# Performance work log

Measured on AMD Instinct MI355X. Metric: run time of the kernel, lower is better.

## Reference

```python
import jax, jax.numpy as jnp
import numpy as np

IN_CH = 768
FH = FW = 14                      # hardcoded feature grid in the module
SCALES = (128.0, 256.0, 512.0)
RATIOS = (0.5, 1.0, 2.0)
A = len(SCALES) * len(RATIOS)     # 9 anchors / location
PRENMS_TOPK = 1000
NMS_THRESH = 0.7
TOPK = 300
MIN_SIZE = 16.0
BBOX_XFORM_CLIP = float(np.log(1000.0 / 16.0))


def generate_anchors(img_h, img_w):
    scales = jnp.asarray(SCALES, jnp.float32)
    ratios = jnp.asarray(RATIOS, jnp.float32)
    h_r = jnp.sqrt(ratios)
    w_r = 1.0 / h_r
    ws = (w_r[:, None] * scales[None, :]).reshape(-1)   # aspect-major, scale-minor
    hs = (h_r[:, None] * scales[None, :]).reshape(-1)
    base = jnp.round(jnp.stack([-ws, -hs, ws, hs], axis=1) / 2.0)  # [A,4]
    stride_h, stride_w = img_h // FH, img_w // FW
    sx = (jnp.arange(FW) * stride_w).astype(jnp.float32)
    sy = (jnp.arange(FH) * stride_h).astype(jnp.float32)
    yy, xx = jnp.meshgrid(sy, sx, indexing='ij')
    shifts = jnp.stack([xx, yy, xx, yy], axis=-1).reshape(-1, 4)   # [H*W,4]
    return (shifts[:, None, :] + base[None, :, :]).reshape(-1, 4)  # [H*W*A,4]


def decode_boxes(deltas, anchors):
    w = anchors[:, 2] - anchors[:, 0]
    h = anchors[:, 3] - anchors[:, 1]
    cx = anchors[:, 0] + 0.5 * w
    cy = anchors[:, 1] + 0.5 * h
    dx, dy = deltas[:, 0], deltas[:, 1]
    dw = jnp.minimum(deltas[:, 2], BBOX_XFORM_CLIP)
    dh = jnp.minimum(deltas[:, 3], BBOX_XFORM_CLIP)
    pcx = dx * w + cx
    pcy = dy * h + cy
    pw = jnp.exp(dw) * w
    ph = jnp.exp(dh) * h
    return jnp.stack([pcx - 0.5 * pw, pcy - 0.5 * ph,
                      pcx + 0.5 * pw, pcy + 0.5 * ph], axis=1)


def nms_keep(boxes, valid, thresh):
    # boxes sorted by descending score; greedy NMS. valid marks boxes that
    # survived the min-size filter.
    area = (boxes[:, 2] - boxes[:, 0]) * (boxes[:, 3] - boxes[:, 1])
    lt = jnp.maximum(boxes[:, None, :2], boxes[None, :, :2])
    rb = jnp.minimum(boxes[:, None, 2:], boxes[None, :, 2:])
    wh = jnp.clip(rb - lt, 0.0)
    inter = wh[..., 0] * wh[..., 1]
    union = area[:, None] + area[None, :] - inter
    iou = jnp.where(union > 0, inter / union, 0.0)   # [N,N]
    n = boxes.shape[0]
    order = jnp.arange(n)

    def body(i, keep):
        sup = (iou[i] > thresh) & keep[i] & (order > i)
        return keep & ~sup

    return jax.lax.fori_loop(0, n, body, valid)


def rpn_forward(image, feature, w_conv, b_conv, w_cls, b_cls, w_reg, b_reg):
    # feature: [1,197,768] -> drop CLS -> raw reshape to [1,768,14,14]
    feat = feature[:, 1:, :].reshape(1, IN_CH, FH, FW)
    x = jax.lax.conv_general_dilated(
        feat, w_conv, window_strides=(1, 1), padding='SAME',
        dimension_numbers=('NCHW', 'OIHW', 'NCHW')) + b_conv[None, :, None, None]
    x = jax.nn.relu(x)
    # 1x1 heads as einsum
    cls = jnp.einsum('nchw,oc->nohw', x, w_cls[:, :, 0, 0]) + b_cls[None, :, None, None]
    reg = jnp.einsum('nchw,oc->nohw', x, w_reg[:, :, 0, 0]) + b_reg[None, :, None, None]
    # [1,A,H,W] -> [H*W*A] (location-major, anchor-minor)
    scores = cls.transpose(0, 2, 3, 1).reshape(-1)
    # [1,4A,H,W] -> [1,A,4,H,W] -> [1,H,W,A,4] -> [H*W*A,4]
    deltas = reg.reshape(1, A, 4, FH, FW).transpose(0, 3, 4, 1, 2).reshape(-1, 4)

    img_h, img_w = image.shape[2], image.shape[3]
    anchors = generate_anchors(img_h, img_w)
    proposals = decode_boxes(deltas, anchors)

    # filter_proposals: sigmoid -> prenms topk -> clip -> min-size -> NMS -> topk
    probs = jax.nn.sigmoid(scores)
    k = min(PRENMS_TOPK, probs.shape[0])
    top_scores, idx = jax.lax.top_k(probs, k)
    boxes = proposals[idx]
    boxes = jnp.stack([jnp.clip(boxes[:, 0], 0.0, img_w),
                       jnp.clip(boxes[:, 1], 0.0, img_h),
                       jnp.clip(boxes[:, 2], 0.0, img_w),
                       jnp.clip(boxes[:, 3], 0.0, img_h)], axis=1)
    ws = boxes[:, 2] - boxes[:, 0]
    hs = boxes[:, 3] - boxes[:, 1]
    valid = (ws >= MIN_SIZE) & (hs >= MIN_SIZE)
    keep = nms_keep(boxes, valid, NMS_THRESH)

    masked = jnp.where(keep, top_scores, -1.0)   # sigmoid scores are > 0
    out_scores, oidx = jax.lax.top_k(masked, TOPK)
    out_boxes = boxes[oidx]
    pad = out_scores > 0.0                        # suppressed slots -> zero pad
    out_boxes = out_boxes * pad[:, None]
    out_scores = out_scores * pad
    return out_boxes, out_scores                  # [TOPK,4], [TOPK]


def setup_inputs() -> dict:
    key = jax.random.key(0)
    ks = jax.random.split(key, 6)
    return {
        'image': jax.random.normal(ks[0], (1, 3, 224, 224), jnp.float32),
        'feature': jax.random.normal(ks[1], (1, 197, IN_CH), jnp.float32),
        'w_conv': 0.01 * jax.random.normal(ks[2], (IN_CH, IN_CH, 3, 3), jnp.float32),
        'b_conv': jnp.zeros((IN_CH,), jnp.float32),
        'w_cls': 0.01 * jax.random.normal(ks[3], (A, IN_CH, 1, 1), jnp.float32),
        'b_cls': jnp.zeros((A,), jnp.float32),
        'w_reg': 0.01 * jax.random.normal(ks[4], (4 * A, IN_CH, 1, 1), jnp.float32),
        'b_reg': jnp.zeros((4 * A,), jnp.float32),
    }


def reference(image, feature, w_conv, b_conv, w_cls, b_cls, w_reg, b_reg):
    return rpn_forward(image, feature, w_conv, b_conv, w_cls, b_cls, w_reg, b_reg)
```

## Files before the change

kernel.cpp:

```cpp
#include <hip/hip_runtime.h>
#include <cstdint>
#include <cstddef>

#define IN_CH 768
#define FH 14
#define FW 14
#define NPOS 196
#define NA 9
#define NANCH 1764
#define K1 1000
#define TOPK_N 300
#define CSPLIT 16
#define CPBLK (IN_CH / CSPLIT)
#define WCH (CPBLK / 4)
#define HQ 8
#define HCC (IN_CH / HQ)
#define BBOX_CLIP 4.135166556742356f
#define IMG_W 224.0f
#define IMG_H 224.0f

typedef unsigned long long ull;

__device__ __forceinline__ uint32_t f2sort(float f) {
    uint32_t b = __float_as_uint(f);
    return (b & 0x80000000u) ? ~b : (b | 0x80000000u);
}
__device__ __forceinline__ float sort2f(uint32_t s) {
    uint32_t b = (s & 0x80000000u) ? (s & 0x7fffffffu) : ~s;
    return __uint_as_float(b);
}
__device__ __forceinline__ ull readlane_u64(ull v, int l) {
    unsigned lo = __builtin_amdgcn_readlane((unsigned)(v & 0xffffffffull), l);
    unsigned hi = __builtin_amdgcn_readlane((unsigned)(v >> 32), l);
    return ((ull)hi << 32) | (ull)lo;
}

__global__ __launch_bounds__(256) void k_pad(const float* __restrict__ feature,
                                             float* __restrict__ pad) {
    const int c = blockIdx.x, t = threadIdx.x;
    const int row = t >> 4, col = t & 15;
    const bool in = (row >= 1 && row <= 14 && col >= 1 && col <= 14);
    pad[(size_t)c * 256 + t] = in ? feature[IN_CH + (size_t)c * NPOS + (row - 1) * FW + (col - 1)] : 0.f;
}

__global__ __launch_bounds__(256) void k_conv(const float* __restrict__ pad,
                                              const float* __restrict__ w_conv,
                                              float* __restrict__ xpart) {
    __shared__ float wlds[CPBLK * 8 * 12];
    const int tid  = threadIdx.x;
    const int wv   = tid >> 6, lane = tid & 63;
    const int cs   = blockIdx.x & (CSPLIT - 1);
    const int ob   = blockIdx.x / CSPLIT;
    const int o0   = ob * 8;

    for (int addr = tid; addr < CPBLK * 8 * 12; addr += 256) {
        const int cc = addr / 96;
        const int r  = addr % 96;
        const int oo = r / 12, k = r % 12;
        float v = 0.f;
        if (k < 9)
            v = w_conv[((size_t)(o0 + oo) * IN_CH + (cs * CPBLK + cc)) * 9 + k];
        wlds[addr] = v;
    }

    const int row = lane >> 2, s4 = (lane & 3) * 4;
    const bool act = (row < FH);
    const int rr = act ? row : 0;

    const int cbase = cs * CPBLK + wv * WCH;
    const float* base = pad + (size_t)cbase * 256 + rr * 16 + s4;

    float acc[8][4];
#pragma unroll
    for (int oo = 0; oo < 8; oo++)
#pragma unroll
        for (int q = 0; q < 4; q++) acc[oo][q] = 0.f;

    float t[3][6];
#pragma unroll
    for (int rI = 0; rI < 3; rI++) {
        const float4 a = *(const float4*)(base + rI * 16);
        const float2 b = *(const float2*)(base + rI * 16 + 4);
        t[rI][0] = a.x; t[rI][1] = a.y; t[rI][2] = a.z; t[rI][3] = a.w;
        t[rI][4] = b.x; t[rI][5] = b.y;
    }

    __syncthreads();

    for (int cc = 0; cc < WCH; cc++) {
        float tn[3][6];
        if (cc + 1 < WCH) {
            const float* nb = base + (size_t)(cc + 1) * 256;
#pragma unroll
            for (int rI = 0; rI < 3; rI++) {
                const float4 a = *(const float4*)(nb + rI * 16);
                const float2 b = *(const float2*)(nb + rI * 16 + 4);
                tn[rI][0] = a.x; tn[rI][1] = a.y; tn[rI][2] = a.z; tn[rI][3] = a.w;
                tn[rI][4] = b.x; tn[rI][5] = b.y;
            }
        }
        const int cib = wv * WCH + cc;
#pragma unroll
        for (int oo = 0; oo < 8; oo++) {
            const int off = (cib * 8 + oo) * 12;
            const float4 wA = *(const float4*)&wlds[off];
            const float4 wB = *(const float4*)&wlds[off + 4];
            const float  w8 = wlds[off + 8];
#pragma unroll
            for (int k = 0; k < 4; k++) {
                acc[oo][k] += t[0][k] * wA.x + t[0][k + 1] * wA.y + t[0][k + 2] * wA.z
                            + t[1][k] * wA.w + t[1][k + 1] * wB.x + t[1][k + 2] * wB.y
                            + t[2][k] * wB.z + t[2][k + 1] * wB.w + t[2][k + 2] * w8;
            }
        }
        if (cc + 1 < WCH) {
#pragma unroll
            for (int rI = 0; rI < 3; rI++)
#pragma unroll
                for (int j = 0; j < 6; j++) t[rI][j] = tn[rI][j];
        }
    }

    __syncthreads();
    float* redbuf = wlds;
    for (int w = 0; w < 4; w++) {
        if (wv == w && act) {
#pragma unroll
            for (int oo = 0; oo < 8; oo++)
#pragma unroll
                for (int k = 0; k < 4; k++) {
                    const int cx = s4 + k;
                    if (cx < FW) {
                        const int p = row * FW + cx;
                        if (w == 0) redbuf[oo * NPOS + p] = acc[oo][k];
                        else        redbuf[oo * NPOS + p] += acc[oo][k];
                    }
                }
        }
        __syncthreads();
    }
    for (int i = tid; i < 8 * NPOS; i += 256)
        xpart[((size_t)cs * IN_CH + o0 + (i / NPOS)) * NPOS + (i % NPOS)] = redbuf[i];
}

__global__ void k_reduce_relu(const float* __restrict__ xpart,
                              const float* __restrict__ b_conv,
                              float* __restrict__ xbuf) {
    const int f = blockIdx.x * blockDim.x + threadIdx.x;
    if (f >= IN_CH * NPOS) return;
    const int o = f / NPOS;
    float s = b_conv[o];
#pragma unroll
    for (int cs = 0; cs < CSPLIT; cs++) s += xpart[(size_t)cs * IN_CH * NPOS + f];
    xbuf[f] = fmaxf(s, 0.f);
}

__global__ __launch_bounds__(256) void k_heads(const float* __restrict__ xbuf,
                                               const float* __restrict__ w_cls,
                                               const float* __restrict__ w_reg,
                                               float* __restrict__ hpart) {
    const int ch = blockIdx.x % 45;
    const int q  = blockIdx.x / 45;
    const int p  = threadIdx.x;
    if (p >= NPOS) return;
    const float* w = (ch < NA) ? (w_cls + (size_t)ch * IN_CH)
                               : (w_reg + (size_t)(ch - NA) * IN_CH);
    float acc = 0.f;
    const int c0 = q * HCC;
#pragma unroll 8
    for (int c = c0; c < c0 + HCC; c++) acc += xbuf[(size_t)c * NPOS + p] * w[c];
    hpart[((size_t)q * 45 + ch) * NPOS + p] = acc;
}

__global__ __launch_bounds__(256) void k_select(const float* __restrict__ hpart,
                                                const float* __restrict__ b_cls,
                                                const float* __restrict__ b_reg,
                                                float* __restrict__ boxes1000,
                                                float* __restrict__ scores1000,
                                                unsigned* __restrict__ invalid) {
    __shared__ ull ks[NANCH];
    __shared__ int prank[4][64];
    const int tid = threadIdx.x;
    const int wv = tid >> 6, lane = tid & 63;

    for (int it = 0; it < 7; it++) {
        const int i = it * 256 + tid;
        if (i < NANCH) {
            const int p = i / NA, a = i % NA;
            float sc = b_cls[a];
#pragma unroll
            for (int q = 0; q < HQ; q++)
                sc += hpart[(size_t)q * 45 * NPOS + (size_t)a * NPOS + p];
            const float prob = 1.0f / (1.0f + expf(-sc));
            ks[i] = ((ull)(__float_as_uint(prob) | 0x80000000u) << 32)
                  | (ull)(0xFFFFFFFFu - (unsigned)i);
        }
    }
    __syncthreads();

    const int cand = blockIdx.x * 64 + lane;
    const ull ki = (cand < NANCH) ? ks[cand] : 0ull;
    int pr = 0;
    const int j0 = wv * 441;
#pragma unroll 7
    for (int j = j0; j < j0 + 441; j++) pr += (ks[j] > ki) ? 1 : 0;
    prank[wv][lane] = pr;
    __syncthreads();

    if (wv == 0 && cand < NANCH) {
        const int rank = prank[0][lane] + prank[1][lane] + prank[2][lane] + prank[3][lane];
        if (rank < K1) {
            const int p = cand / NA, a = cand % NA;
            const int yy = p / FW, xx = p % FW;
            const int r = a / 3, s = a % 3;
            const float scv = (s == 0) ? 128.f : ((s == 1) ? 256.f : 512.f);
            const float rat = (r == 0) ? 0.5f : ((r == 1) ? 1.0f : 2.0f);
            const float hr = sqrtf(rat), wr = 1.0f / hr;
            const float wsv = wr * scv, hsv = hr * scv;
            const float sxf = (float)(xx * 16), syf = (float)(yy * 16);
            const float ax0 = sxf + rintf(-0.5f * wsv);
            const float ay0 = syf + rintf(-0.5f * hsv);
            const float ax1 = sxf + rintf(0.5f * wsv);
            const float ay1 = syf + rintf(0.5f * hsv);
            const float w = ax1 - ax0, h = ay1 - ay0;
            const float cx = ax0 + 0.5f * w, cy = ay0 + 0.5f * h;
            const int rc0 = NA + (a * 4 + 0), rc1 = NA + (a * 4 + 1);
            const int rc2 = NA + (a * 4 + 2), rc3 = NA + (a * 4 + 3);
            float dx = b_reg[a * 4 + 0], dy = b_reg[a * 4 + 1];
            float dwv = b_reg[a * 4 + 2], dhv = b_reg[a * 4 + 3];
#pragma unroll
            for (int q = 0; q < HQ; q++) {
                const size_t base = (size_t)q * 45 * NPOS;
                dx  += hpart[base + (size_t)rc0 * NPOS + p];
                dy  += hpart[base + (size_t)rc1 * NPOS + p];
                dwv += hpart[base + (size_t)rc2 * NPOS + p];
                dhv += hpart[base + (size_t)rc3 * NPOS + p];
            }
            const float dw = fminf(dwv, BBOX_CLIP);
            const float dh = fminf(dhv, BBOX_CLIP);
            const float pcx = dx * w + cx, pcy = dy * h + cy;
            const float pw = expf(dw) * w, ph = expf(dh) * h;
            const float b0 = fminf(fmaxf(pcx - 0.5f * pw, 0.f), IMG_W);
            const float b1 = fminf(fmaxf(pcy - 0.5f * ph, 0.f), IMG_H);
            const float b2 = fminf(fmaxf(pcx + 0.5f * pw, 0.f), IMG_W);
            const float b3 = fminf(fmaxf(pcy + 0.5f * ph, 0.f), IMG_H);
            boxes1000[rank * 4 + 0] = b0; boxes1000[rank * 4 + 1] = b1;
            boxes1000[rank * 4 + 2] = b2; boxes1000[rank * 4 + 3] = b3;
            scores1000[rank] = __uint_as_float((unsigned)(ki >> 32) & 0x7FFFFFFFu);
            const float bw = b2 - b0, bh = b3 - b1;
            invalid[rank] = (bw >= 16.f && bh >= 16.f) ? 0u : 1u;
        }
    }
}

__global__ __launch_bounds__(1024) void k_iou_mask(const float* __restrict__ boxes1000,
                                                   ull* __restrict__ mask) {
    const int i = blockIdx.x;
    const int j = threadIdx.x;
    const float ix0 = boxes1000[i * 4 + 0], iy0 = boxes1000[i * 4 + 1];
    const float ix1 = boxes1000[i * 4 + 2], iy1 = boxes1000[i * 4 + 3];
    const float areai = (ix1 - ix0) * (iy1 - iy0);
    bool pred = false;
    if (j < K1 && j > i) {
        const float jx0 = boxes1000[j * 4 + 0], jy0 = boxes1000[j * 4 + 1];
        const float jx1 = boxes1000[j * 4 + 2], jy1 = boxes1000[j * 4 + 3];
        const float areaj = (jx1 - jx0) * (jy1 - jy0);
        const float xx0 = fmaxf(ix0, jx0), yy0 = fmaxf(iy0, jy0);
        const float xx1 = fminf(ix1, jx1), yy1 = fminf(iy1, jy1);
        const float w = fmaxf(xx1 - xx0, 0.f), h = fmaxf(yy1 - yy0, 0.f);
        const float inter = w * h;
        const float uni = areai + areaj - inter;
        const float iou = (uni > 0.f) ? inter / uni : 0.f;
        pred = iou > 0.7f;
    }
    const ull m = __ballot(pred);
    if ((j & 63) == 0) mask[(size_t)i * 16 + (j >> 6)] = m;
}

__global__ __launch_bounds__(64) void k_scan(const ull* __restrict__ mask,
                                             const unsigned* __restrict__ invalid,
                                             ull* __restrict__ remw_g) {
    const int lane = threadIdx.x;

    unsigned invpack = 0u;
#pragma unroll
    for (int w = 0; w < 16; w++) {
        const int idx = w * 64 + lane;
        const unsigned iv = (idx < K1) ? (invalid[idx] & 1u) : 0u;
        invpack |= iv << w;
    }

    ull col[2][16];
    col[0][0] = mask[(size_t)lane * 16 + 0];
#pragma unroll
    for (int q = 0; q < 2; q++) {
        const int row = q * 64 + lane;
        col[1][q] = mask[(size_t)row * 16 + 1];
    }

    unsigned keptpack = 0u;
    ull cur = __ballot((invpack >> 0) & 1u);
    ull remv_store = 0ull;

#pragma unroll
    for (int w = 0; w < 16; w++) {
        const int par = w & 1;
        ull kept = 0ull;
#pragma unroll
        for (int b = 0; b < 64; b++) {
            const ull db = readlane_u64(col[par][w], b);
            const bool kb = (w * 64 + b < K1) && (((cur >> b) & 1ull) == 0ull);
            cur  |= kb ? db : 0ull;
            kept |= kb ? (1ull << b) : 0ull;
        }
        remv_store = (lane == w) ? cur : remv_store;
        keptpack |= (unsigned)((kept >> lane) & 1ull) << w;

        if (w + 1 < 16) {
            const int np = par ^ 1;
            if (w + 2 < 16) {
#pragma unroll
                for (int q = 0; q < 16; q++) {
                    if (q <= w + 2) {
                        const int row = q * 64 + lane;
                        col[par][q] = mask[(size_t)((row < K1) ? row : (K1 - 1)) * 16 + (w + 2)];
                    }
                }
            }
            ull contrib = 0ull;
#pragma unroll
            for (int q = 0; q < 16; q++) {
                if (q <= w) {
                    const bool kb = (keptpack >> q) & 1u;
                    contrib |= kb ? col[np][q] : 0ull;
                }
            }
#pragma unroll
            for (int off = 1; off < 64; off <<= 1)
                contrib |= __shfl_xor(contrib, off);
            cur = __ballot((invpack >> (w + 1)) & 1u) | readlane_u64(contrib, 0);
        }
    }
    if (lane < 16) remw_g[lane] = remv_store;
}

__global__ __launch_bounds__(256) void k_out(const ull* __restrict__ remw_g,
                                             const float* __restrict__ scores1000,
                                             const float* __restrict__ boxes1000,
                                             float* __restrict__ out) {
    __shared__ ull ks[1024];
    __shared__ int prank[4][64];
    const int tid = threadIdx.x;
    const int wv = tid >> 6, lane = tid & 63;

    for (int it = 0; it < 4; it++) {
        const int t = it * 256 + tid;
        const ull w = remw_g[t >> 6];
        ull k = 0ull;
        if (t < K1) {
            const bool rem = (w >> (t & 63)) & 1ull;
            const float m = rem ? -1.0f : scores1000[t];
            k = ((ull)f2sort(m) << 32) | (ull)(0xFFFFFFFFu - (unsigned)t);
        }
        ks[t] = k;
    }
    __syncthreads();

    const int cand = blockIdx.x * 64 + lane;
    const ull kj = (cand < K1) ? ks[cand] : 0ull;
    int pr = 0;
    const int j0 = wv * 250;
#pragma unroll 10
    for (int j = j0; j < j0 + 250; j++) pr += (ks[j] > kj) ? 1 : 0;
    prank[wv][lane] = pr;
    __syncthreads();

    if (wv == 0 && cand < K1) {
        const int rank = prank[0][lane] + prank[1][lane] + prank[2][lane] + prank[3][lane];
        if (rank < TOPK_N) {
            const float sc = sort2f((unsigned)(kj >> 32));
            const unsigned b = 0xFFFFFFFFu - (unsigned)(kj & 0xFFFFFFFFull);
            float o0 = 0.f, o1 = 0.f, o2 = 0.f, o3 = 0.f, os = 0.f;
            if (sc > 0.f) {
                o0 = boxes1000[b * 4 + 0]; o1 = boxes1000[b * 4 + 1];
                o2 = boxes1000[b * 4 + 2]; o3 = boxes1000[b * 4 + 3];
                os = sc;
            }
            out[rank * 4 + 0] = o0; out[rank * 4 + 1] = o1;
            out[rank * 4 + 2] = o2; out[rank * 4 + 3] = o3;
            out[1200 + rank] = os;
        }
    }
}

extern "C" void kernel_launch(void* const* d_in, const int* in_sizes, int n_in,
                              void* d_out, int out_size, void* d_ws, size_t ws_size,
                              hipStream_t stream) {
    const float* feature = (const float*)d_in[1];
    const float* w_conv  = (const float*)d_in[2];
    const float* b_conv  = (const float*)d_in[3];
    const float* w_cls   = (const float*)d_in[4];
    const float* b_cls   = (const float*)d_in[5];
    const float* w_reg   = (const float*)d_in[6];
    const float* b_reg   = (const float*)d_in[7];
    float* out = (float*)d_out;

    char* w = (char*)d_ws;
    float*    pad     = (float*)(w + 0);
    float*    xpart   = (float*)(w + 786432);
    float*    xbuf    = (float*)(w + 10420224);
    float*    hpart   = (float*)(w + 11022336);
    float*    boxes   = (float*)(w + 11304576);
    float*    scrs    = (float*)(w + 11320576);
    unsigned* inval   = (unsigned*)(w + 11324576);
    ull*      mask    = (ull*)  (w + 11328576);
    ull*      remw    = (ull*)  (w + 11456576);

    k_pad<<<IN_CH, 256, 0, stream>>>(feature, pad);
    k_conv<<<96 * CSPLIT, 256, 0, stream>>>(pad, w_conv, xpart);
    k_reduce_relu<<<(IN_CH * NPOS + 255) / 256, 256, 0, stream>>>(xpart, b_conv, xbuf);
    k_heads<<<45 * HQ, 256, 0, stream>>>(xbuf, w_cls, w_reg, hpart);
    k_select<<<28, 256, 0, stream>>>(hpart, b_cls, b_reg, boxes, scrs, inval);
    k_iou_mask<<<K1, 1024, 0, stream>>>(boxes, mask);
    k_scan<<<1, 64, 0, stream>>>(mask, inval, remw);
    k_out<<<16, 256, 0, stream>>>(remw, scrs, boxes, out);
}
```

Before: 197.7 us.

## Fuse split-K reduce into conv via atomic counter, merge scan and output kernels

The conv kernel now bumps a per-output-block atomic counter after writing its partial sums, and the last of the split blocks to finish does the bias, reduce and ReLU itself, so the separate reduce kernel is no longer needed. The NMS scan and top-k output kernels become one 1024-thread block that hands the removal mask through shared memory. Both rank computations switch from serial LDS compare loops to register-held keys counted with ballot and popcount. This removes two kernel launches and their global round-trips, at the cost of an extra memset, threadfence and atomic overhead, and a single-block output stage.

```diff
diff --git a/kernel.cpp b/kernel.cpp
--- a/kernel.cpp
+++ b/kernel.cpp
@@ -45,8 +45,12 @@
 
 __global__ __launch_bounds__(256) void k_conv(const float* __restrict__ pad,
                                               const float* __restrict__ w_conv,
-                                              float* __restrict__ xpart) {
+                                              const float* __restrict__ b_conv,
+                                              float* __restrict__ xpart,
+                                              float* __restrict__ xbuf,
+                                              unsigned* __restrict__ cnt) {
     __shared__ float wlds[CPBLK * 8 * 12];
+    __shared__ unsigned done;
     const int tid  = threadIdx.x;
     const int wv   = tid >> 6, lane = tid & 63;
     const int cs   = blockIdx.x & (CSPLIT - 1);
@@ -141,18 +145,21 @@
     }
     for (int i = tid; i < 8 * NPOS; i += 256)
         xpart[((size_t)cs * IN_CH + o0 + (i / NPOS)) * NPOS + (i % NPOS)] = redbuf[i];
-}
-
-__global__ void k_reduce_relu(const float* __restrict__ xpart,
-                              const float* __restrict__ b_conv,
-                              float* __restrict__ xbuf) {
-    const int f = blockIdx.x * blockDim.x + threadIdx.x;
-    if (f >= IN_CH * NPOS) return;
-    const int o = f / NPOS;
-    float s = b_conv[o];
-#pragma unroll
-    for (int cs = 0; cs < CSPLIT; cs++) s += xpart[(size_t)cs * IN_CH * NPOS + f];
-    xbuf[f] = fmaxf(s, 0.f);
+
+    __threadfence();
+    if (tid == 0) done = atomicAdd(&cnt[ob], 1u);
+    __syncthreads();
+    if (done == (unsigned)(CSPLIT - 1)) {
+        __threadfence();
+        for (int i = tid; i < 8 * NPOS; i += 256) {
+            const int o = o0 + i / NPOS, p = i % NPOS;
+            float s = b_conv[o];
+#pragma unroll
+            for (int cs2 = 0; cs2 < CSPLIT; cs2++)
+                s += xpart[((size_t)cs2 * IN_CH + o) * NPOS + p];
+            xbuf[(size_t)o * NPOS + p] = fmaxf(s, 0.f);
+        }
+    }
 }
 
 __global__ __launch_bounds__(256) void k_heads(const float* __restrict__ xbuf,
@@ -179,7 +186,7 @@
                                                 float* __restrict__ scores1000,
                                                 unsigned* __restrict__ invalid) {
     __shared__ ull ks[NANCH];
-    __shared__ int prank[4][64];
+    __shared__ int rankbuf[64];
     const int tid = threadIdx.x;
     const int wv = tid >> 6, lane = tid & 63;
 
@@ -198,17 +205,27 @@
     }
     __syncthreads();
 
+    ull kreg[28];
+#pragma unroll
+    for (int q = 0; q < 28; q++) {
+        const int idx = q * 64 + lane;
+        kreg[q] = (idx < NANCH) ? ks[idx] : 0ull;
+    }
+
+    for (int cl = wv * 16; cl < wv * 16 + 16; cl++) {
+        const ull cand = ks[(blockIdx.x * 64 + cl < NANCH) ? (blockIdx.x * 64 + cl) : 0];
+        int r = 0;
+#pragma unroll
+        for (int q = 0; q < 28; q++)
+            r += __popcll(__ballot(kreg[q] > cand));
+        if (lane == 0) rankbuf[cl] = r;
+    }
+    __syncthreads();
+
     const int cand = blockIdx.x * 64 + lane;
-    const ull ki = (cand < NANCH) ? ks[cand] : 0ull;
-    int pr = 0;
-    const int j0 = wv * 441;
-#pragma unroll 7
-    for (int j = j0; j < j0 + 441; j++) pr += (ks[j] > ki) ? 1 : 0;
-    prank[wv][lane] = pr;
-    __syncthreads();
-
     if (wv == 0 && cand < NANCH) {
-        const int rank = prank[0][lane] + prank[1][lane] + prank[2][lane] + prank[3][lane];
+        const ull ki = ks[cand];
+        const int rank = rankbuf[lane];
         if (rank < K1) {
             const int p = cand / NA, a = cand % NA;
             const int yy = p / FW, xx = p % FW;
@@ -277,88 +294,85 @@
     if ((j & 63) == 0) mask[(size_t)i * 16 + (j >> 6)] = m;
 }
 
-__global__ __launch_bounds__(64) void k_scan(const ull* __restrict__ mask,
-                                             const unsigned* __restrict__ invalid,
-                                             ull* __restrict__ remw_g) {
-    const int lane = threadIdx.x;
-
-    unsigned invpack = 0u;
-#pragma unroll
-    for (int w = 0; w < 16; w++) {
-        const int idx = w * 64 + lane;
-        const unsigned iv = (idx < K1) ? (invalid[idx] & 1u) : 0u;
-        invpack |= iv << w;
-    }
-
-    ull col[2][16];
-    col[0][0] = mask[(size_t)lane * 16 + 0];
-#pragma unroll
-    for (int q = 0; q < 2; q++) {
-        const int row = q * 64 + lane;
-        col[1][q] = mask[(size_t)row * 16 + 1];
-    }
-
-    unsigned keptpack = 0u;
-    ull cur = __ballot((invpack >> 0) & 1u);
-    ull remv_store = 0ull;
-
-#pragma unroll
-    for (int w = 0; w < 16; w++) {
-        const int par = w & 1;
-        ull kept = 0ull;
-#pragma unroll
-        for (int b = 0; b < 64; b++) {
-            const ull db = readlane_u64(col[par][w], b);
-            const bool kb = (w * 64 + b < K1) && (((cur >> b) & 1ull) == 0ull);
-            cur  |= kb ? db : 0ull;
-            kept |= kb ? (1ull << b) : 0ull;
-        }
-        remv_store = (lane == w) ? cur : remv_store;
-        keptpack |= (unsigned)((kept >> lane) & 1ull) << w;
-
-        if (w + 1 < 16) {
-            const int np = par ^ 1;
-            if (w + 2 < 16) {
-#pragma unroll
-                for (int q = 0; q < 16; q++) {
-                    if (q <= w + 2) {
-                        const int row = q * 64 + lane;
-                        col[par][q] = mask[(size_t)((row < K1) ? row : (K1 - 1)) * 16 + (w + 2)];
+__global__ __launch_bounds__(1024) void k_scanout(const ull* __restrict__ mask,
+                                                  const unsigned* __restrict__ invalid,
+                                                  const float* __restrict__ scores1000,
+                                                  const float* __restrict__ boxes1000,
+                                                  float* __restrict__ out) {
+    __shared__ ull ks[1024];
+    __shared__ ull remw_s[16];
+    const int tid = threadIdx.x;
+    const int wv = tid >> 6, lane = tid & 63;
+
+    if (wv == 0) {
+        unsigned invpack = 0u;
+#pragma unroll
+        for (int w = 0; w < 16; w++) {
+            const int idx = w * 64 + lane;
+            const unsigned iv = (idx < K1) ? (invalid[idx] & 1u) : 0u;
+            invpack |= iv << w;
+        }
+
+        ull col[2][16];
+        col[0][0] = mask[(size_t)lane * 16 + 0];
+#pragma unroll
+        for (int q = 0; q < 2; q++) {
+            const int row = q * 64 + lane;
+            col[1][q] = mask[(size_t)row * 16 + 1];
+        }
+
+        unsigned keptpack = 0u;
+        ull cur = __ballot((invpack >> 0) & 1u);
+        ull remv_store = 0ull;
+
+#pragma unroll
+        for (int w = 0; w < 16; w++) {
+            const int par = w & 1;
+            ull kept = 0ull;
+#pragma unroll
+            for (int b = 0; b < 64; b++) {
+                const ull db = readlane_u64(col[par][w], b);
+                const bool kb = (w * 64 + b < K1) && (((cur >> b) & 1ull) == 0ull);
+                cur  |= kb ? db : 0ull;
+                kept |= kb ? (1ull << b) : 0ull;
+            }
+            remv_store = (lane == w) ? cur : remv_store;
+            keptpack |= (unsigned)((kept >> lane) & 1ull) << w;
+
+            if (w + 1 < 16) {
+                const int np = par ^ 1;
+                if (w + 2 < 16) {
+#pragma unroll
+                    for (int q = 0; q < 16; q++) {
+                        if (q <= w + 2) {
+                            const int row = q * 64 + lane;
+                            col[par][q] = mask[(size_t)((row < K1) ? row : (K1 - 1)) * 16 + (w + 2)];
+                        }
                     }
                 }
+                ull contrib = 0ull;
+#pragma unroll
+                for (int q = 0; q < 16; q++) {
+                    if (q <= w) {
+                        const bool kb = (keptpack >> q) & 1u;
+                        contrib |= kb ? col[np][q] : 0ull;
+                    }
+                }
+#pragma unroll
+                for (int off = 1; off < 64; off <<= 1)
+                    contrib |= __shfl_xor(contrib, off);
+                cur = __ballot((invpack >> (w + 1)) & 1u) | readlane_u64(contrib, 0);
             }
-            ull contrib = 0ull;
-#pragma unroll
-            for (int q = 0; q < 16; q++) {
-                if (q <= w) {
-                    const bool kb = (keptpack >> q) & 1u;
-                    contrib |= kb ? col[np][q] : 0ull;
-                }
-            }
-#pragma unroll
-            for (int off = 1; off < 64; off <<= 1)
-                contrib |= __shfl_xor(contrib, off);
-            cur = __ballot((invpack >> (w + 1)) & 1u) | readlane_u64(contrib, 0);
-        }
-    }
-    if (lane < 16) remw_g[lane] = remv_store;
-}
-
-__global__ __launch_bounds__(256) void k_out(const ull* __restrict__ remw_g,
-                                             const float* __restrict__ scores1000,
-                                             const float* __restrict__ boxes1000,
-                                             float* __restrict__ out) {
-    __shared__ ull ks[1024];
-    __shared__ int prank[4][64];
-    const int tid = threadIdx.x;
-    const int wv = tid >> 6, lane = tid & 63;
-
-    for (int it = 0; it < 4; it++) {
-        const int t = it * 256 + tid;
-        const ull w = remw_g[t >> 6];
+        }
+        if (lane < 16) remw_s[lane] = remv_store;
+    }
+    __syncthreads();
+
+    {
+        const int t = tid;
         ull k = 0ull;
         if (t < K1) {
-            const bool rem = (w >> (t & 63)) & 1ull;
+            const bool rem = (remw_s[t >> 6] >> (t & 63)) & 1ull;
             const float m = rem ? -1.0f : scores1000[t];
             k = ((ull)f2sort(m) << 32) | (ull)(0xFFFFFFFFu - (unsigned)t);
         }
@@ -366,30 +380,34 @@
     }
     __syncthreads();
 
-    const int cand = blockIdx.x * 64 + lane;
-    const ull kj = (cand < K1) ? ks[cand] : 0ull;
-    int pr = 0;
-    const int j0 = wv * 250;
-#pragma unroll 10
-    for (int j = j0; j < j0 + 250; j++) pr += (ks[j] > kj) ? 1 : 0;
-    prank[wv][lane] = pr;
-    __syncthreads();
-
-    if (wv == 0 && cand < K1) {
-        const int rank = prank[0][lane] + prank[1][lane] + prank[2][lane] + prank[3][lane];
-        if (rank < TOPK_N) {
-            const float sc = sort2f((unsigned)(kj >> 32));
-            const unsigned b = 0xFFFFFFFFu - (unsigned)(kj & 0xFFFFFFFFull);
-            float o0 = 0.f, o1 = 0.f, o2 = 0.f, o3 = 0.f, os = 0.f;
-            if (sc > 0.f) {
-                o0 = boxes1000[b * 4 + 0]; o1 = boxes1000[b * 4 + 1];
-                o2 = boxes1000[b * 4 + 2]; o3 = boxes1000[b * 4 + 3];
-                os = sc;
-            }
-            out[rank * 4 + 0] = o0; out[rank * 4 + 1] = o1;
-            out[rank * 4 + 2] = o2; out[rank * 4 + 3] = o3;
-            out[1200 + rank] = os;
-        }
+    ull kreg[16];
+#pragma unroll
+    for (int q = 0; q < 16; q++) kreg[q] = ks[q * 64 + lane];
+
+    int myrank = K1;
+    for (int cl = 0; cl < 64; cl++) {
+        const ull cand = ks[wv * 64 + cl];
+        int r = 0;
+#pragma unroll
+        for (int q = 0; q < 16; q++)
+            r += __popcll(__ballot(kreg[q] > cand));
+        if (lane == cl) myrank = r;
+    }
+
+    const int c = tid;
+    const ull kj = ks[c];
+    if (c < K1 && myrank < TOPK_N) {
+        const float sc = sort2f((unsigned)(kj >> 32));
+        const unsigned b = 0xFFFFFFFFu - (unsigned)(kj & 0xFFFFFFFFull);
+        float o0 = 0.f, o1 = 0.f, o2 = 0.f, o3 = 0.f, os = 0.f;
+        if (sc > 0.f) {
+            o0 = boxes1000[b * 4 + 0]; o1 = boxes1000[b * 4 + 1];
+            o2 = boxes1000[b * 4 + 2]; o3 = boxes1000[b * 4 + 3];
+            os = sc;
+        }
+        out[myrank * 4 + 0] = o0; out[myrank * 4 + 1] = o1;
+        out[myrank * 4 + 2] = o2; out[myrank * 4 + 3] = o3;
+        out[1200 + myrank] = os;
     }
 }
 
@@ -414,14 +432,13 @@
     float*    scrs    = (float*)(w + 11320576);
     unsigned* inval   = (unsigned*)(w + 11324576);
     ull*      mask    = (ull*)  (w + 11328576);
-    ull*      remw    = (ull*)  (w + 11456576);
-
+    unsigned* cnt     = (unsigned*)(w + 11456576);
+
+    hipMemsetAsync((void*)cnt, 0, 96 * sizeof(unsigned), stream);
     k_pad<<<IN_CH, 256, 0, stream>>>(feature, pad);
-    k_conv<<<96 * CSPLIT, 256, 0, stream>>>(pad, w_conv, xpart);
-    k_reduce_relu<<<(IN_CH * NPOS + 255) / 256, 256, 0, stream>>>(xpart, b_conv, xbuf);
+    k_conv<<<96 * CSPLIT, 256, 0, stream>>>(pad, w_conv, b_conv, xpart, xbuf, cnt);
     k_heads<<<45 * HQ, 256, 0, stream>>>(xbuf, w_cls, w_reg, hpart);
     k_select<<<28, 256, 0, stream>>>(hpart, b_cls, b_reg, boxes, scrs, inval);
     k_iou_mask<<<K1, 1024, 0, stream>>>(boxes, mask);
-    k_scan<<<1, 64, 0, stream>>>(mask, inval, remw);
-    k_out<<<16, 256, 0, stream>>>(remw, scrs, boxes, out);
-}
+    k_scanout<<<1, 1024, 0, stream>>>(mask, inval, scrs, boxes, out);
+}
```

After: 402.4 us. +103.6%, slower.
